# Optimization experiments

Measured on AMD Instinct MI355X. Metric: run time of the kernel, lower is better.

Reference implementation:

```python
import jax, jax.numpy as jnp
import numpy as np

N_NODES = 100000
N_EDGES = 1600000


def gcn_conv(x, W, b, src, dst, n):
    # PyG GCNConv: x @ W, add self-loops, symmetric deg^{-1/2} normalization,
    # sum-aggregate messages from src into dst, then add bias.
    h = x @ W  # [N, out]
    loops = jnp.arange(n, dtype=src.dtype)
    s = jnp.concatenate([src, loops])
    d = jnp.concatenate([dst, loops])
    deg = jax.ops.segment_sum(jnp.ones_like(d, dtype=h.dtype), d, num_segments=n)
    dinv = 1.0 / jnp.sqrt(deg)  # deg >= 1 thanks to self-loops
    norm = dinv[s] * dinv[d]  # [E + N]
    msg = h[s] * norm[:, None]
    out = jax.ops.segment_sum(msg, d, num_segments=n)
    return out + b


def setup_inputs() -> dict:
    key = jax.random.key(0)
    k1, k2, k3, k4 = jax.random.split(key, 4)
    x = jax.random.normal(k1, (N_NODES, 64), dtype=jnp.float32)
    edge_index = jax.random.randint(k2, (2, N_EDGES), 0, N_NODES, dtype=jnp.int64)
    W1 = jax.random.normal(k3, (64, 32), dtype=jnp.float32) * (1.0 / np.sqrt(64))
    b1 = jnp.zeros((32,), dtype=jnp.float32)
    W2 = jax.random.normal(k4, (32, 16), dtype=jnp.float32) * (1.0 / np.sqrt(32))
    b2 = jnp.zeros((16,), dtype=jnp.float32)
    return {"x": x, "edge_index": edge_index, "W1": W1, "b1": b1, "W2": W2, "b2": b2}


def reference(x, edge_index, W1, b1, W2, b2):
    n = x.shape[0]
    src, dst = edge_index[0], edge_index[1]
    h = gcn_conv(x, W1, b1, src, dst, n)
    h = jax.nn.relu(h)
    h = gcn_conv(h, W2, b2, src, dst, n)
    return jax.nn.log_softmax(h, axis=1)
```

## Files before the change

### kernel.cpp

```cpp
#include <hip/hip_runtime.h>
#include <hip/hip_bf16.h>


#define FEAT_IN 64
#define FEAT_H  32
#define FEAT_O  16
#define MAXNB   512
#define PART_G  192

__device__ __forceinline__ float2 upk_bf2(unsigned w) {
    return make_float2(__uint_as_float(w << 16), __uint_as_float(w & 0xFFFF0000u));
}

__global__ void k_detect(const uint4* __restrict__ xw4,
                         const int* __restrict__ ei, int* __restrict__ flags) {
    __shared__ int s_f32, s_i64nz;
    if (threadIdx.x == 0) { s_f32 = 0; s_i64nz = 0; }
    __syncthreads();
    int t = threadIdx.x;
    int hit = 0;
    for (int i = t; i < 4096; i += 256) {
        uint4 u = xw4[i];
        unsigned a0 = u.x, a1 = u.y, a2 = u.z, a3 = u.w;
        if ((a0 & 0x7F800000u) == 0x7F800000u || (a0 & 0x00007F80u) == 0x00007F80u) hit = 1;
        if ((a1 & 0x7F800000u) == 0x7F800000u || (a1 & 0x00007F80u) == 0x00007F80u) hit = 1;
        if ((a2 & 0x7F800000u) == 0x7F800000u || (a2 & 0x00007F80u) == 0x00007F80u) hit = 1;
        if ((a3 & 0x7F800000u) == 0x7F800000u || (a3 & 0x00007F80u) == 0x00007F80u) hit = 1;
    }
    if (hit) atomicOr(&s_f32, 1);
    int nz = 0;
    for (int i = t; i < 128; i += 256) {
        if (ei[2 * i + 1] != 0) nz = 1;
    }
    if (nz) atomicOr(&s_i64nz, 1);
    __syncthreads();
    if (t == 0) { flags[0] = s_f32; flags[1] = s_i64nz ? 0 : 1; }
}

__global__ void k_hist(const int* __restrict__ ei, int e, const int* __restrict__ flags,
                       int* __restrict__ hist, int G, int NBk) {
    __shared__ int lh[MAXNB];
    int t = threadIdx.x, g = blockIdx.x;
    for (int i = t; i < NBk; i += 256) lh[i] = 0;
    __syncthreads();
    int chunk = (e + G - 1) / G;
    int beg = g * chunk, end = min(e, beg + chunk);
    bool i64 = flags[1] != 0;
    for (int i = beg + t; i < end; i += 256) {
        int d = i64 ? ei[2 * (e + i)] : ei[e + i];
        atomicAdd(&lh[d >> 8], 1);
    }
    __syncthreads();
    for (int i = t; i < NBk; i += 256) hist[(size_t)i * G + g] = lh[i];
}

__global__ void k_scan1(const int* __restrict__ in, int* __restrict__ out,
                        int* __restrict__ bsum, int len) {
    __shared__ int s[256];
    int t = threadIdx.x;
    int base = blockIdx.x * 1024 + t * 4;
    int a0 = (base + 0) < len ? in[base + 0] : 0;
    int a1 = (base + 1) < len ? in[base + 1] : 0;
    int a2 = (base + 2) < len ? in[base + 2] : 0;
    int a3 = (base + 3) < len ? in[base + 3] : 0;
    int tsum = a0 + a1 + a2 + a3;
    s[t] = tsum;
    __syncthreads();
    for (int off = 1; off < 256; off <<= 1) {
        int x = (t >= off) ? s[t - off] : 0;
        __syncthreads();
        s[t] += x;
        __syncthreads();
    }
    int ex = s[t] - tsum;
    if (base + 0 < len) out[base + 0] = ex;
    if (base + 1 < len) out[base + 1] = ex + a0;
    if (base + 2 < len) out[base + 2] = ex + a0 + a1;
    if (base + 3 < len) out[base + 3] = ex + a0 + a1 + a2;
    if (t == 255) bsum[blockIdx.x] = s[255];
}

__global__ void k_scan2(int* __restrict__ bsum, int nb) {
    __shared__ int s[256];
    int t = threadIdx.x;
    int v = (t < nb) ? bsum[t] : 0;
    s[t] = v;
    __syncthreads();
    for (int off = 1; off < 256; off <<= 1) {
        int x = (t >= off) ? s[t - off] : 0;
        __syncthreads();
        s[t] += x;
        __syncthreads();
    }
    if (t < nb) bsum[t] = s[t] - v;
}

__device__ __forceinline__ int base_at(const int* base, const int* bsum, int idx) {
    return base[idx] + bsum[idx >> 10];
}

__global__ void k_partition(const int* __restrict__ ei, int e, const int* __restrict__ flags,
                            const int* __restrict__ base, const int* __restrict__ bsum,
                            int* __restrict__ part, int G, int NBk) {
    __shared__ int cur[MAXNB];
    int t = threadIdx.x, g = blockIdx.x;
    for (int i = t; i < NBk; i += 256) cur[i] = base_at(base, bsum, i * G + g);
    __syncthreads();
    int chunk = (e + G - 1) / G;
    int beg = g * chunk, end = min(e, beg + chunk);
    bool i64 = flags[1] != 0;
    for (int i = beg + t; i < end; i += 256) {
        int s, d;
        if (i64) { s = ei[2 * i]; d = ei[2 * (e + i)]; }
        else     { s = ei[i];     d = ei[e + i]; }
        int pos = atomicAdd(&cur[d >> 8], 1);
        part[pos] = s | ((d & 255) << 24);
    }
}

__global__ void k_bucket_csr(const int* __restrict__ part, const int* __restrict__ base,
                             const int* __restrict__ bsum, int e, int G, int NBk, int n,
                             int* __restrict__ row_start, int* __restrict__ col,
                             float* __restrict__ dinv) {
    __shared__ int cnt[256], spre[256], cur[256], ssc[256];
    int t = threadIdx.x, b = blockIdx.x;
    int beg = base_at(base, bsum, b * G);
    int end = (b == NBk - 1) ? e : base_at(base, bsum, (b + 1) * G);
    cnt[t] = 0; cur[t] = 0;
    __syncthreads();
    for (int j = beg + t; j < end; j += 256) atomicAdd(&cnt[((unsigned)part[j]) >> 24], 1);
    __syncthreads();
    int v = cnt[t];
    ssc[t] = v;
    __syncthreads();
    for (int off = 1; off < 256; off <<= 1) {
        int x = (t >= off) ? ssc[t - off] : 0;
        __syncthreads();
        ssc[t] += x;
        __syncthreads();
    }
    spre[t] = ssc[t] - v;
    int node = b * 256 + t;
    if (node < n) {
        row_start[node] = beg + spre[t];
        dinv[node] = rsqrtf((float)v + 1.0f);
    }
    if (b == NBk - 1 && t == 0) row_start[n] = e;
    __syncthreads();
    for (int j = beg + t; j < end; j += 256) {
        int r = part[j];
        int dl = ((unsigned)r) >> 24;
        int off = atomicAdd(&cur[dl], 1);
        col[beg + spre[dl] + off] = r & 0x00FFFFFF;
    }
}

__global__ void k_gemm1(const void* __restrict__ xv, const void* __restrict__ W1v,
                        const int* __restrict__ flags, const float* __restrict__ dinv,
                        __hip_bfloat162* __restrict__ h1s2, int n) {
    __shared__ float sW[FEAT_IN * FEAT_H];
    __shared__ float sx[16][FEAT_IN + 1];
    int t = threadIdx.x;
    bool f32 = flags[0] != 0;
    if (f32) {
        const float* W = (const float*)W1v;
        for (int i = t; i < FEAT_IN * FEAT_H; i += 256) sW[i] = W[i];
    } else {
        const __hip_bfloat16* W = (const __hip_bfloat16*)W1v;
        for (int i = t; i < FEAT_IN * FEAT_H; i += 256) sW[i] = __bfloat162float(W[i]);
    }
#pragma unroll
    for (int tile = 0; tile < 2; ++tile) {
        int nodeBase = blockIdx.x * 32 + tile * 16;
        __syncthreads();
        {
            int xn = t >> 4, c = t & 15;
            int node = nodeBase + xn;
            if (node < n) {
                if (f32) {
                    float4 v = ((const float4*)xv)[(size_t)node * 16 + c];
                    sx[xn][c * 4 + 0] = v.x; sx[xn][c * 4 + 1] = v.y;
                    sx[xn][c * 4 + 2] = v.z; sx[xn][c * 4 + 3] = v.w;
                } else {
                    const __hip_bfloat162* x2 = (const __hip_bfloat162*)xv;
                    float2 a = __bfloat1622float2(x2[(size_t)node * 32 + c * 2 + 0]);
                    float2 b = __bfloat1622float2(x2[(size_t)node * 32 + c * 2 + 1]);
                    sx[xn][c * 4 + 0] = a.x; sx[xn][c * 4 + 1] = a.y;
                    sx[xn][c * 4 + 2] = b.x; sx[xn][c * 4 + 3] = b.y;
                }
            }
        }
        __syncthreads();
        int nl = t >> 4, g = t & 15;
        int node = nodeBase + nl;
        if (node < n) {
            float a0 = 0.0f, a1 = 0.0f;
#pragma unroll
            for (int k = 0; k < FEAT_IN; ++k) {
                float s = sx[nl][k];
                a0 += s * sW[k * FEAT_H + 2 * g];
                a1 += s * sW[k * FEAT_H + 2 * g + 1];
            }
            float dv = dinv[node];
            __hip_bfloat162 o;
            o.x = __float2bfloat16(a0 * dv);
            o.y = __float2bfloat16(a1 * dv);
            h1s2[(size_t)node * 16 + g] = o;
        }
    }
}

__global__ void k_gather1_gemm2(const int* __restrict__ row_start, const int* __restrict__ col,
                                const uint4* __restrict__ h1q, const void* __restrict__ W2v,
                                const void* __restrict__ b1v, const int* __restrict__ flags,
                                const float* __restrict__ dinv,
                                __hip_bfloat162* __restrict__ h2s2, int n) {
    __shared__ float sW[FEAT_H * FEAT_O];
    __shared__ float sb1[FEAT_H];
    __shared__ float sz[64][FEAT_H + 1];
    int t = threadIdx.x;
    bool f32 = flags[0] != 0;
    if (f32) {
        const float* W = (const float*)W2v;
        for (int i = t; i < FEAT_H * FEAT_O; i += 256) sW[i] = W[i];
        if (t < FEAT_H) sb1[t] = ((const float*)b1v)[t];
    } else {
        const __hip_bfloat16* W = (const __hip_bfloat16*)W2v;
        for (int i = t; i < FEAT_H * FEAT_O; i += 256) sW[i] = __bfloat162float(W[i]);
        if (t < FEAT_H) sb1[t] = __bfloat162float(((const __hip_bfloat16*)b1v)[t]);
    }
    __syncthreads();

    int g = t >> 2, l = t & 3;
    int d = blockIdx.x * 64 + g;
    if (d < n) {
        float a[8];
        {
            uint4 u = h1q[(size_t)d * 4 + l];
            float2 p0 = upk_bf2(u.x), p1 = upk_bf2(u.y), p2 = upk_bf2(u.z), p3 = upk_bf2(u.w);
            a[0] = p0.x; a[1] = p0.y; a[2] = p1.x; a[3] = p1.y;
            a[4] = p2.x; a[5] = p2.y; a[6] = p3.x; a[7] = p3.y;
        }
        int beg = row_start[d], end = row_start[d + 1];
        int j = beg;
        for (; j + 4 <= end; j += 4) {
            int c0 = col[j + 0], c1 = col[j + 1], c2 = col[j + 2], c3 = col[j + 3];
            uint4 u0 = h1q[(size_t)c0 * 4 + l];
            uint4 u1 = h1q[(size_t)c1 * 4 + l];
            uint4 u2 = h1q[(size_t)c2 * 4 + l];
            uint4 u3 = h1q[(size_t)c3 * 4 + l];
            float2 p;
            p = upk_bf2(u0.x); a[0] += p.x; a[1] += p.y;
            p = upk_bf2(u0.y); a[2] += p.x; a[3] += p.y;
            p = upk_bf2(u0.z); a[4] += p.x; a[5] += p.y;
            p = upk_bf2(u0.w); a[6] += p.x; a[7] += p.y;
            p = upk_bf2(u1.x); a[0] += p.x; a[1] += p.y;
            p = upk_bf2(u1.y); a[2] += p.x; a[3] += p.y;
            p = upk_bf2(u1.z); a[4] += p.x; a[5] += p.y;
            p = upk_bf2(u1.w); a[6] += p.x; a[7] += p.y;
            p = upk_bf2(u2.x); a[0] += p.x; a[1] += p.y;
            p = upk_bf2(u2.y); a[2] += p.x; a[3] += p.y;
            p = upk_bf2(u2.z); a[4] += p.x; a[5] += p.y;
            p = upk_bf2(u2.w); a[6] += p.x; a[7] += p.y;
            p = upk_bf2(u3.x); a[0] += p.x; a[1] += p.y;
            p = upk_bf2(u3.y); a[2] += p.x; a[3] += p.y;
            p = upk_bf2(u3.z); a[4] += p.x; a[5] += p.y;
            p = upk_bf2(u3.w); a[6] += p.x; a[7] += p.y;
        }
        for (; j < end; ++j) {
            uint4 u = h1q[(size_t)col[j] * 4 + l];
            float2 p;
            p = upk_bf2(u.x); a[0] += p.x; a[1] += p.y;
            p = upk_bf2(u.y); a[2] += p.x; a[3] += p.y;
            p = upk_bf2(u.z); a[4] += p.x; a[5] += p.y;
            p = upk_bf2(u.w); a[6] += p.x; a[7] += p.y;
        }
        float dv = dinv[d];
#pragma unroll
        for (int k = 0; k < 8; ++k)
            sz[g][l * 8 + k] = fmaxf(dv * a[k] + sb1[l * 8 + k], 0.0f);
    }
    __syncthreads();
#pragma unroll
    for (int it = 0; it < 2; ++it) {
        int nl = (t >> 3) + it * 32;
        int m = t & 7;
        int node = blockIdx.x * 64 + nl;
        if (node < n) {
            float a0 = 0.0f, a1 = 0.0f;
#pragma unroll
            for (int f = 0; f < FEAT_H; ++f) {
                float z = sz[nl][f];
                a0 += z * sW[f * FEAT_O + 2 * m];
                a1 += z * sW[f * FEAT_O + 2 * m + 1];
            }
            float dv = dinv[node];
            __hip_bfloat162 o;
            o.x = __float2bfloat16(a0 * dv);
            o.y = __float2bfloat16(a1 * dv);
            h2s2[(size_t)node * 8 + m] = o;
        }
    }
}

__global__ void k_gather2_lsm(const int* __restrict__ row_start, const int* __restrict__ col,
                              const uint4* __restrict__ h2q, const void* __restrict__ b2v,
                              const int* __restrict__ flags, const float* __restrict__ dinv,
                              float4* __restrict__ out4, int n) {
    __shared__ float sb2[FEAT_O];
    int t = threadIdx.x;
    if (t < FEAT_O) {
        sb2[t] = flags[0] ? ((const float*)b2v)[t]
                          : __bfloat162float(((const __hip_bfloat16*)b2v)[t]);
    }
    __syncthreads();
    int g = t >> 1, h = t & 1;
    int d = blockIdx.x * 128 + g;
    if (d >= n) return;
    float a[8];
    {
        uint4 u = h2q[(size_t)d * 2 + h];
        float2 p0 = upk_bf2(u.x), p1 = upk_bf2(u.y), p2 = upk_bf2(u.z), p3 = upk_bf2(u.w);
        a[0] = p0.x; a[1] = p0.y; a[2] = p1.x; a[3] = p1.y;
        a[4] = p2.x; a[5] = p2.y; a[6] = p3.x; a[7] = p3.y;
    }
    int beg = row_start[d], end = row_start[d + 1];
    int j = beg;
    for (; j + 4 <= end; j += 4) {
        int c0 = col[j + 0], c1 = col[j + 1], c2 = col[j + 2], c3 = col[j + 3];
        uint4 u0 = h2q[(size_t)c0 * 2 + h];
        uint4 u1 = h2q[(size_t)c1 * 2 + h];
        uint4 u2 = h2q[(size_t)c2 * 2 + h];
        uint4 u3 = h2q[(size_t)c3 * 2 + h];
        float2 p;
        p = upk_bf2(u0.x); a[0] += p.x; a[1] += p.y;
        p = upk_bf2(u0.y); a[2] += p.x; a[3] += p.y;
        p = upk_bf2(u0.z); a[4] += p.x; a[5] += p.y;
        p = upk_bf2(u0.w); a[6] += p.x; a[7] += p.y;
        p = upk_bf2(u1.x); a[0] += p.x; a[1] += p.y;
        p = upk_bf2(u1.y); a[2] += p.x; a[3] += p.y;
        p = upk_bf2(u1.z); a[4] += p.x; a[5] += p.y;
        p = upk_bf2(u1.w); a[6] += p.x; a[7] += p.y;
        p = upk_bf2(u2.x); a[0] += p.x; a[1] += p.y;
        p = upk_bf2(u2.y); a[2] += p.x; a[3] += p.y;
        p = upk_bf2(u2.z); a[4] += p.x; a[5] += p.y;
        p = upk_bf2(u2.w); a[6] += p.x; a[7] += p.y;
        p = upk_bf2(u3.x); a[0] += p.x; a[1] += p.y;
        p = upk_bf2(u3.y); a[2] += p.x; a[3] += p.y;
        p = upk_bf2(u3.z); a[4] += p.x; a[5] += p.y;
        p = upk_bf2(u3.w); a[6] += p.x; a[7] += p.y;
    }
    for (; j < end; ++j) {
        uint4 u = h2q[(size_t)col[j] * 2 + h];
        float2 p;
        p = upk_bf2(u.x); a[0] += p.x; a[1] += p.y;
        p = upk_bf2(u.y); a[2] += p.x; a[3] += p.y;
        p = upk_bf2(u.z); a[4] += p.x; a[5] += p.y;
        p = upk_bf2(u.w); a[6] += p.x; a[7] += p.y;
    }
    float dv = dinv[d];
    float v[8];
    float mx = -1e30f;
#pragma unroll
    for (int k = 0; k < 8; ++k) {
        v[k] = dv * a[k] + sb2[h * 8 + k];
        mx = fmaxf(mx, v[k]);
    }
    mx = fmaxf(mx, __shfl_xor(mx, 1));
    float ssum = 0.0f;
#pragma unroll
    for (int k = 0; k < 8; ++k) ssum += __expf(v[k] - mx);
    ssum += __shfl_xor(ssum, 1);
    float lg = mx + logf(ssum);
    float4 o0 = { v[0] - lg, v[1] - lg, v[2] - lg, v[3] - lg };
    float4 o1 = { v[4] - lg, v[5] - lg, v[6] - lg, v[7] - lg };
    out4[(size_t)d * 4 + h * 2 + 0] = o0;
    out4[(size_t)d * 4 + h * 2 + 1] = o1;
}

extern "C" void kernel_launch(void* const* d_in, const int* in_sizes, int n_in,
                              void* d_out, int out_size, void* d_ws, size_t ws_size,
                              hipStream_t stream) {
    const void* x  = d_in[0];
    const int*  ei = (const int*)d_in[1];
    const void* W1 = d_in[2];
    const void* b1 = d_in[3];
    const void* W2 = d_in[4];
    const void* b2 = d_in[5];

    const int n = in_sizes[0] / FEAT_IN;
    const int e = in_sizes[1] / 2;
    const int NBk = (n + 255) >> 8;
    const int G = PART_G;
    const int hlen = NBk * G;

    int* part = (int*)d_ws;
    __hip_bfloat162* h1s2 = (__hip_bfloat162*)d_ws;
    int* col  = (int*)d_ws + e;
    __hip_bfloat162* h2s2 = (__hip_bfloat162*)(col + e);
    float* dinv = (float*)(h2s2 + 8 * (size_t)n);
    int* flags     = (int*)(dinv + n);
    int* hist      = flags + 4;
    int* base      = hist + hlen;
    int* bsum      = base + hlen;
    int* row_start = bsum + 256;

    k_detect<<<1, 256, 0, stream>>>((const uint4*)x, ei, flags);

    k_hist<<<G, 256, 0, stream>>>(ei, e, flags, hist, G, NBk);
    int snb = (hlen + 1023) / 1024;
    k_scan1<<<snb, 256, 0, stream>>>(hist, base, bsum, hlen);
    k_scan2<<<1, 256, 0, stream>>>(bsum, snb);
    k_partition<<<G, 256, 0, stream>>>(ei, e, flags, base, bsum, part, G, NBk);
    k_bucket_csr<<<NBk, 256, 0, stream>>>(part, base, bsum, e, G, NBk, n,
                                          row_start, col, dinv);

    k_gemm1<<<(n + 31) / 32, 256, 0, stream>>>(x, W1, flags, dinv, h1s2, n);
    k_gather1_gemm2<<<(n + 63) / 64, 256, 0, stream>>>(row_start, col, (const uint4*)h1s2,
                                                       W2, b1, flags, dinv, h2s2, n);
    k_gather2_lsm<<<(n + 127) / 128, 256, 0, stream>>>(row_start, col, (const uint4*)h2s2,
                                                       b2, flags, dinv, (float4*)d_out, n);
}
```

Before: 197.7 us.

## Drop dtype-detect kernel, fold block-sum scan into consumers, widen partition grid

```diff
diff --git a/kernel.cpp b/kernel.cpp
--- a/kernel.cpp
+++ b/kernel.cpp
@@ -6,38 +6,14 @@
 #define FEAT_H  32
 #define FEAT_O  16
 #define MAXNB   512
-#define PART_G  192
+#define PART_G  256
+#define MAXSNB  128
 
 __device__ __forceinline__ float2 upk_bf2(unsigned w) {
     return make_float2(__uint_as_float(w << 16), __uint_as_float(w & 0xFFFF0000u));
 }
 
-__global__ void k_detect(const uint4* __restrict__ xw4,
-                         const int* __restrict__ ei, int* __restrict__ flags) {
-    __shared__ int s_f32, s_i64nz;
-    if (threadIdx.x == 0) { s_f32 = 0; s_i64nz = 0; }
-    __syncthreads();
-    int t = threadIdx.x;
-    int hit = 0;
-    for (int i = t; i < 4096; i += 256) {
-        uint4 u = xw4[i];
-        unsigned a0 = u.x, a1 = u.y, a2 = u.z, a3 = u.w;
-        if ((a0 & 0x7F800000u) == 0x7F800000u || (a0 & 0x00007F80u) == 0x00007F80u) hit = 1;
-        if ((a1 & 0x7F800000u) == 0x7F800000u || (a1 & 0x00007F80u) == 0x00007F80u) hit = 1;
-        if ((a2 & 0x7F800000u) == 0x7F800000u || (a2 & 0x00007F80u) == 0x00007F80u) hit = 1;
-        if ((a3 & 0x7F800000u) == 0x7F800000u || (a3 & 0x00007F80u) == 0x00007F80u) hit = 1;
-    }
-    if (hit) atomicOr(&s_f32, 1);
-    int nz = 0;
-    for (int i = t; i < 128; i += 256) {
-        if (ei[2 * i + 1] != 0) nz = 1;
-    }
-    if (nz) atomicOr(&s_i64nz, 1);
-    __syncthreads();
-    if (t == 0) { flags[0] = s_f32; flags[1] = s_i64nz ? 0 : 1; }
-}
-
-__global__ void k_hist(const int* __restrict__ ei, int e, const int* __restrict__ flags,
+__global__ void k_hist(const int* __restrict__ dst, int e,
                        int* __restrict__ hist, int G, int NBk) {
     __shared__ int lh[MAXNB];
     int t = threadIdx.x, g = blockIdx.x;
@@ -45,11 +21,7 @@
     __syncthreads();
     int chunk = (e + G - 1) / G;
     int beg = g * chunk, end = min(e, beg + chunk);
-    bool i64 = flags[1] != 0;
-    for (int i = beg + t; i < end; i += 256) {
-        int d = i64 ? ei[2 * (e + i)] : ei[e + i];
-        atomicAdd(&lh[d >> 8], 1);
-    }
+    for (int i = beg + t; i < end; i += 256) atomicAdd(&lh[dst[i] >> 8], 1);
     __syncthreads();
     for (int i = t; i < NBk; i += 256) hist[(size_t)i * G + g] = lh[i];
 }
@@ -80,52 +52,50 @@
     if (t == 255) bsum[blockIdx.x] = s[255];
 }
 
-__global__ void k_scan2(int* __restrict__ bsum, int nb) {
-    __shared__ int s[256];
-    int t = threadIdx.x;
-    int v = (t < nb) ? bsum[t] : 0;
-    s[t] = v;
-    __syncthreads();
-    for (int off = 1; off < 256; off <<= 1) {
-        int x = (t >= off) ? s[t - off] : 0;
-        __syncthreads();
-        s[t] += x;
-        __syncthreads();
-    }
-    if (t < nb) bsum[t] = s[t] - v;
-}
-
-__device__ __forceinline__ int base_at(const int* base, const int* bsum, int idx) {
-    return base[idx] + bsum[idx >> 10];
-}
-
-__global__ void k_partition(const int* __restrict__ ei, int e, const int* __restrict__ flags,
+__device__ __forceinline__ void scan_bsum(const int* __restrict__ bsum, int snb,
+                                          int* __restrict__ sps, int t) {
+    if (t < snb) sps[t] = bsum[t];
+    __syncthreads();
+    if (t == 0) {
+        int acc = 0;
+        for (int i = 0; i < snb; ++i) { int v = sps[i]; sps[i] = acc; acc += v; }
+    }
+    __syncthreads();
+}
+
+__global__ void k_partition(const int* __restrict__ src, const int* __restrict__ dst, int e,
                             const int* __restrict__ base, const int* __restrict__ bsum,
-                            int* __restrict__ part, int G, int NBk) {
+                            int snb, int* __restrict__ part, int G, int NBk) {
     __shared__ int cur[MAXNB];
+    __shared__ int sps[MAXSNB];
     int t = threadIdx.x, g = blockIdx.x;
-    for (int i = t; i < NBk; i += 256) cur[i] = base_at(base, bsum, i * G + g);
+    scan_bsum(bsum, snb, sps, t);
+    for (int i = t; i < NBk; i += 256) {
+        size_t idx = (size_t)i * G + g;
+        cur[i] = base[idx] + sps[idx >> 10];
+    }
     __syncthreads();
     int chunk = (e + G - 1) / G;
     int beg = g * chunk, end = min(e, beg + chunk);
-    bool i64 = flags[1] != 0;
     for (int i = beg + t; i < end; i += 256) {
-        int s, d;
-        if (i64) { s = ei[2 * i]; d = ei[2 * (e + i)]; }
-        else     { s = ei[i];     d = ei[e + i]; }
-        int pos = atomicAdd(&cur[d >> 8], 1);
-        part[pos] = s | ((d & 255) << 24);
+        int s_ = src[i], d_ = dst[i];
+        int pos = atomicAdd(&cur[d_ >> 8], 1);
+        part[pos] = s_ | ((d_ & 255) << 24);
     }
 }
 
 __global__ void k_bucket_csr(const int* __restrict__ part, const int* __restrict__ base,
-                             const int* __restrict__ bsum, int e, int G, int NBk, int n,
-                             int* __restrict__ row_start, int* __restrict__ col,
+                             const int* __restrict__ bsum, int snb, int e, int G, int NBk,
+                             int n, int* __restrict__ row_start, int* __restrict__ col,
                              float* __restrict__ dinv) {
     __shared__ int cnt[256], spre[256], cur[256], ssc[256];
+    __shared__ int sps[MAXSNB];
     int t = threadIdx.x, b = blockIdx.x;
-    int beg = base_at(base, bsum, b * G);
-    int end = (b == NBk - 1) ? e : base_at(base, bsum, (b + 1) * G);
+    scan_bsum(bsum, snb, sps, t);
+    size_t ib = (size_t)b * G;
+    size_t ie = (size_t)(b + 1) * G;
+    int beg = base[ib] + sps[ib >> 10];
+    int end = (b == NBk - 1) ? e : (base[ie] + sps[ie >> 10]);
     cnt[t] = 0; cur[t] = 0;
     __syncthreads();
     for (int j = beg + t; j < end; j += 256) atomicAdd(&cnt[((unsigned)part[j]) >> 24], 1);
@@ -155,20 +125,13 @@
     }
 }
 
-__global__ void k_gemm1(const void* __restrict__ xv, const void* __restrict__ W1v,
-                        const int* __restrict__ flags, const float* __restrict__ dinv,
+__global__ void k_gemm1(const float* __restrict__ x, const float* __restrict__ W1,
+                        const float* __restrict__ dinv,
                         __hip_bfloat162* __restrict__ h1s2, int n) {
     __shared__ float sW[FEAT_IN * FEAT_H];
     __shared__ float sx[16][FEAT_IN + 1];
     int t = threadIdx.x;
-    bool f32 = flags[0] != 0;
-    if (f32) {
-        const float* W = (const float*)W1v;
-        for (int i = t; i < FEAT_IN * FEAT_H; i += 256) sW[i] = W[i];
-    } else {
-        const __hip_bfloat16* W = (const __hip_bfloat16*)W1v;
-        for (int i = t; i < FEAT_IN * FEAT_H; i += 256) sW[i] = __bfloat162float(W[i]);
-    }
+    for (int i = t; i < FEAT_IN * FEAT_H; i += 256) sW[i] = W1[i];
 #pragma unroll
     for (int tile = 0; tile < 2; ++tile) {
         int nodeBase = blockIdx.x * 32 + tile * 16;
@@ -177,17 +140,9 @@
             int xn = t >> 4, c = t & 15;
             int node = nodeBase + xn;
             if (node < n) {
-                if (f32) {
-                    float4 v = ((const float4*)xv)[(size_t)node * 16 + c];
-                    sx[xn][c * 4 + 0] = v.x; sx[xn][c * 4 + 1] = v.y;
-                    sx[xn][c * 4 + 2] = v.z; sx[xn][c * 4 + 3] = v.w;
-                } else {
-                    const __hip_bfloat162* x2 = (const __hip_bfloat162*)xv;
-                    float2 a = __bfloat1622float2(x2[(size_t)node * 32 + c * 2 + 0]);
-                    float2 b = __bfloat1622float2(x2[(size_t)node * 32 + c * 2 + 1]);
-                    sx[xn][c * 4 + 0] = a.x; sx[xn][c * 4 + 1] = a.y;
-                    sx[xn][c * 4 + 2] = b.x; sx[xn][c * 4 + 3] = b.y;
-                }
+                float4 v = ((const float4*)x)[(size_t)node * 16 + c];
+                sx[xn][c * 4 + 0] = v.x; sx[xn][c * 4 + 1] = v.y;
+                sx[xn][c * 4 + 2] = v.z; sx[xn][c * 4 + 3] = v.w;
             }
         }
         __syncthreads();
@@ -211,24 +166,16 @@
 }
 
 __global__ void k_gather1_gemm2(const int* __restrict__ row_start, const int* __restrict__ col,
-                                const uint4* __restrict__ h1q, const void* __restrict__ W2v,
-                                const void* __restrict__ b1v, const int* __restrict__ flags,
+                                const uint4* __restrict__ h1q, const float* __restrict__ W2,
+                                const float* __restrict__ b1,
                                 const float* __restrict__ dinv,
                                 __hip_bfloat162* __restrict__ h2s2, int n) {
     __shared__ float sW[FEAT_H * FEAT_O];
     __shared__ float sb1[FEAT_H];
     __shared__ float sz[64][FEAT_H + 1];
     int t = threadIdx.x;
-    bool f32 = flags[0] != 0;
-    if (f32) {
-        const float* W = (const float*)W2v;
-        for (int i = t; i < FEAT_H * FEAT_O; i += 256) sW[i] = W[i];
-        if (t < FEAT_H) sb1[t] = ((const float*)b1v)[t];
-    } else {
-        const __hip_bfloat16* W = (const __hip_bfloat16*)W2v;
-        for (int i = t; i < FEAT_H * FEAT_O; i += 256) sW[i] = __bfloat162float(W[i]);
-        if (t < FEAT_H) sb1[t] = __bfloat162float(((const __hip_bfloat16*)b1v)[t]);
-    }
+    for (int i = t; i < FEAT_H * FEAT_O; i += 256) sW[i] = W2[i];
+    if (t < FEAT_H) sb1[t] = b1[t];
     __syncthreads();
 
     int g = t >> 2, l = t & 3;
@@ -237,9 +184,11 @@
         float a[8];
         {
             uint4 u = h1q[(size_t)d * 4 + l];
-            float2 p0 = upk_bf2(u.x), p1 = upk_bf2(u.y), p2 = upk_bf2(u.z), p3 = upk_bf2(u.w);
-            a[0] = p0.x; a[1] = p0.y; a[2] = p1.x; a[3] = p1.y;
-            a[4] = p2.x; a[5] = p2.y; a[6] = p3.x; a[7] = p3.y;
+            float2 p;
+            p = upk_bf2(u.x); a[0] = p.x; a[1] = p.y;
+            p = upk_bf2(u.y); a[2] = p.x; a[3] = p.y;
+            p = upk_bf2(u.z); a[4] = p.x; a[5] = p.y;
+            p = upk_bf2(u.w); a[6] = p.x; a[7] = p.y;
         }
         int beg = row_start[d], end = row_start[d + 1];
         int j = beg;
@@ -304,15 +253,12 @@
 }
 
 __global__ void k_gather2_lsm(const int* __restrict__ row_start, const int* __restrict__ col,
-                              const uint4* __restrict__ h2q, const void* __restrict__ b2v,
-                              const int* __restrict__ flags, const float* __restrict__ dinv,
+                              const uint4* __restrict__ h2q, const float* __restrict__ b2,
+                              const float* __restrict__ dinv,
                               float4* __restrict__ out4, int n) {
     __shared__ float sb2[FEAT_O];
     int t = threadIdx.x;
-    if (t < FEAT_O) {
-        sb2[t] = flags[0] ? ((const float*)b2v)[t]
-                          : __bfloat162float(((const __hip_bfloat16*)b2v)[t]);
-    }
+    if (t < FEAT_O) sb2[t] = b2[t];
     __syncthreads();
     int g = t >> 1, h = t & 1;
     int d = blockIdx.x * 128 + g;
@@ -320,9 +266,11 @@
     float a[8];
     {
         uint4 u = h2q[(size_t)d * 2 + h];
-        float2 p0 = upk_bf2(u.x), p1 = upk_bf2(u.y), p2 = upk_bf2(u.z), p3 = upk_bf2(u.w);
-        a[0] = p0.x; a[1] = p0.y; a[2] = p1.x; a[3] = p1.y;
-        a[4] = p2.x; a[5] = p2.y; a[6] = p3.x; a[7] = p3.y;
+        float2 p;
+        p = upk_bf2(u.x); a[0] = p.x; a[1] = p.y;
+        p = upk_bf2(u.y); a[2] = p.x; a[3] = p.y;
+        p = upk_bf2(u.z); a[4] = p.x; a[5] = p.y;
+        p = upk_bf2(u.w); a[6] = p.x; a[7] = p.y;
     }
     int beg = row_start[d], end = row_start[d + 1];
     int j = beg;
@@ -381,43 +329,41 @@
 extern "C" void kernel_launch(void* const* d_in, const int* in_sizes, int n_in,
                               void* d_out, int out_size, void* d_ws, size_t ws_size,
                               hipStream_t stream) {
-    const void* x  = d_in[0];
-    const int*  ei = (const int*)d_in[1];
-    const void* W1 = d_in[2];
-    const void* b1 = d_in[3];
-    const void* W2 = d_in[4];
-    const void* b2 = d_in[5];
+    const float* x  = (const float*)d_in[0];
+    const int*   ei = (const int*)d_in[1];
+    const float* W1 = (const float*)d_in[2];
+    const float* b1 = (const float*)d_in[3];
+    const float* W2 = (const float*)d_in[4];
+    const float* b2 = (const float*)d_in[5];
 
     const int n = in_sizes[0] / FEAT_IN;
     const int e = in_sizes[1] / 2;
+    const int* src = ei;
+    const int* dst = ei + e;
     const int NBk = (n + 255) >> 8;
     const int G = PART_G;
     const int hlen = NBk * G;
+    const int snb = (hlen + 1023) / 1024;
 
     int* part = (int*)d_ws;
     __hip_bfloat162* h1s2 = (__hip_bfloat162*)d_ws;
     int* col  = (int*)d_ws + e;
     __hip_bfloat162* h2s2 = (__hip_bfloat162*)(col + e);
     float* dinv = (float*)(h2s2 + 8 * (size_t)n);
-    int* flags     = (int*)(dinv + n);
-    int* hist      = flags + 4;
+    int* hist      = (int*)(dinv + n);
     int* base      = hist + hlen;
     int* bsum      = base + hlen;
-    int* row_start = bsum + 256;
-
-    k_detect<<<1, 256, 0, stream>>>((const uint4*)x, ei, flags);
-
-    k_hist<<<G, 256, 0, stream>>>(ei, e, flags, hist, G, NBk);
-    int snb = (hlen + 1023) / 1024;
+    int* row_start = bsum + MAXSNB;
+
+    k_hist<<<G, 256, 0, stream>>>(dst, e, hist, G, NBk);
     k_scan1<<<snb, 256, 0, stream>>>(hist, base, bsum, hlen);
-    k_scan2<<<1, 256, 0, stream>>>(bsum, snb);
-    k_partition<<<G, 256, 0, stream>>>(ei, e, flags, base, bsum, part, G, NBk);
-    k_bucket_csr<<<NBk, 256, 0, stream>>>(part, base, bsum, e, G, NBk, n,
+    k_partition<<<G, 256, 0, stream>>>(src, dst, e, base, bsum, snb, part, G, NBk);
+    k_bucket_csr<<<NBk, 256, 0, stream>>>(part, base, bsum, snb, e, G, NBk, n,
                                           row_start, col, dinv);
 
-    k_gemm1<<<(n + 31) / 32, 256, 0, stream>>>(x, W1, flags, dinv, h1s2, n);
+    k_gemm1<<<(n + 31) / 32, 256, 0, stream>>>(x, W1, dinv, h1s2, n);
     k_gather1_gemm2<<<(n + 63) / 64, 256, 0, stream>>>(row_start, col, (const uint4*)h1s2,
-                                                       W2, b1, flags, dinv, h2s2, n);
+                                                       W2, b1, dinv, h2s2, n);
     k_gather2_lsm<<<(n + 127) / 128, 256, 0, stream>>>(row_start, col, (const uint4*)h2s2,
-                                                       b2, flags, dinv, (float4*)d_out, n);
-}
+                                                       b2, dinv, (float4*)d_out, n);
+}
```

Result: faster. 184.2 us (-6.8%).
